# Kernel tuning notes

Measured on AMD Instinct MI355X. Metric: run time of the kernel, lower is better.

## Reference

```python
import jax, jax.numpy as jnp
import numpy as np

B, S, D = 8, 2048, 512  # batch, seq_len, input_dim == qk_dim
K_SIZE = 6


def setup_inputs() -> dict:
    key = jax.random.key(0)
    ks = jax.random.split(key, 8)
    return {
        "evo_local": jax.random.normal(ks[0], (B, S, D), dtype=jnp.float32),
        "Wq": jax.random.normal(ks[1], (D, D), dtype=jnp.float32) * (1.0 / np.sqrt(D)),
        "bq": jax.random.normal(ks[2], (D,), dtype=jnp.float32) * 0.02,
        "dw_w": jax.random.normal(ks[3], (D, 1, K_SIZE), dtype=jnp.float32) * 0.1,  # depthwise conv (O, I/groups=1, K)
        "dw_b": jax.random.normal(ks[4], (D,), dtype=jnp.float32) * 0.02,
        "pw_w": jax.random.normal(ks[5], (D, D), dtype=jnp.float32) * (1.0 / np.sqrt(D)),  # pointwise 1x1 conv as matrix
        "pw_b": jax.random.normal(ks[6], (D,), dtype=jnp.float32) * 0.02,
        "pos": jax.random.normal(ks[7], (1, S, D), dtype=jnp.float32),
    }


def reference(evo_local, Wq, bq, dw_w, dw_b, pw_w, pw_b, pos):
    d = evo_local.shape[-1]
    # Q = Linear(evo_local) + learned positional encoding
    Q = jnp.einsum("bsd,ed->bse", evo_local, Wq) + bq + pos  # [B,S,D]

    # depthwise conv1d, kernel=6, torch padding='same' for even kernel -> pad (2, 3)
    x = jnp.transpose(evo_local, (0, 2, 1))  # [B,D,S]
    kv = jax.lax.conv_general_dilated(
        x, dw_w,
        window_strides=(1,),
        padding=[(2, 3)],
        feature_group_count=d,
        dimension_numbers=("NCH", "OIH", "NCH"),
    ) + dw_b[None, :, None]  # [B,D,S]
    # pointwise 1x1 conv
    kv = jnp.einsum("od,bds->bos", pw_w, kv) + pw_b[None, :, None]  # [B,D,S]
    KV = jnp.transpose(kv, (0, 2, 1))  # [B,S,D]; K and V share this

    scale = 1.0 / jnp.sqrt(jnp.float32(d))
    scores = jnp.einsum("bsd,btd->bst", Q, KV) * scale  # [B,S,S]
    attn = jax.nn.softmax(scores, axis=-1)
    out = jnp.einsum("bst,btd->bsd", attn, KV)
    return out + KV + evo_local
```

## Files before the change

kernel.cpp:

```cpp
#include <hip/hip_runtime.h>


typedef unsigned short ushort_t;
typedef __attribute__((ext_vector_type(8))) short short8;
typedef __attribute__((ext_vector_type(8))) unsigned short u16x8;
typedef __attribute__((ext_vector_type(4))) float f32x4;
typedef float4 f4;

__device__ __forceinline__ float bf2f(ushort_t h) {
    union { unsigned u; float f; } v; v.u = ((unsigned)h) << 16; return v.f;
}
__device__ __forceinline__ ushort_t f2bf(float f) {
    union { float f; unsigned u; } v; v.f = f;
    unsigned r = (v.u + 0x7FFFu + ((v.u >> 16) & 1u)) >> 16;
    return (ushort_t)r;
}

__device__ __forceinline__ void gld_lds16(const void* g, void* l) {
    __builtin_amdgcn_global_load_lds((const __attribute__((address_space(1))) void*)g,
                                     (__attribute__((address_space(3))) void*)l, 16, 0, 0);
}

#define BAR()   asm volatile("s_barrier" ::: "memory")
#define WAITV8  do { asm volatile("s_waitcnt vmcnt(8)" ::: "memory"); __builtin_amdgcn_sched_barrier(0); } while (0)
#define WAITV0  do { asm volatile("s_waitcnt vmcnt(0)" ::: "memory"); __builtin_amdgcn_sched_barrier(0); } while (0)
#define WAITL   do { asm volatile("s_waitcnt lgkmcnt(0)" ::: "memory"); __builtin_amdgcn_sched_barrier(0); } while (0)

template<int EPI>
__global__ __launch_bounds__(512, 2)
void mfma_nt256(const ushort_t* __restrict__ A, long long sA, int ldA,
                const ushort_t* __restrict__ B, long long sB, int ldB,
                int N, int K, float alpha,
                ushort_t* __restrict__ Ch, long long sC,
                float* __restrict__ Cf,
                const ushort_t* __restrict__ addH, const ushort_t* __restrict__ addL,
                const float* __restrict__ addF, long long sAdd)
{
    __shared__ __align__(16) ushort_t lds[65536];

    const int t = threadIdx.x;
    const int w = t >> 6, lane = t & 63;
    const int z = blockIdx.z;
    A += (long long)z * sA;
    B += (long long)z * sB;
    const int m0 = blockIdx.y * 256, n0 = blockIdx.x * 256;
    const int wr = w >> 2, wc = w & 3;
    const int fr = lane & 15, kg = lane >> 4;
    const int nkt = K >> 6;

    const int sRo = lane >> 2;
    const long long sCk = ((lane & 3) ^ ((lane >> 3) & 3)) * 8;
    const int co = (kg ^ ((fr >> 1) & 3)) * 8;

#define STAGE(P, base0, ld, segbase, h, Ts) do {                                         \
    const long long kk_ = (long long)(((Ts) < nkt ? (Ts) : (nkt - 1)) * 64 + (h) * 32) + sCk; \
    const int g0_ = w * 2;                                                               \
    gld_lds16((P) + (long long)((base0) + g0_ * 16 + sRo) * (ld) + kk_,                  \
              &lds[(segbase) + g0_ * 512]);                                              \
    gld_lds16((P) + (long long)((base0) + g0_ * 16 + 16 + sRo) * (ld) + kk_,             \
              &lds[(segbase) + g0_ * 512 + 512]);                                        \
} while (0)

#define AREAD(ksseg) do {                                                                \
    const int ab_ = (ksseg) * 8192 + wr * 4096 + fr * 32 + co;                           \
    _Pragma("unroll") for (int fm_ = 0; fm_ < 8; ++fm_)                                  \
        afr[fm_] = *(const short8*)&lds[ab_ + fm_ * 512];                                \
} while (0)

#define BREAD(ksseg, fnh) do {                                                           \
    const int bb_ = 32768 + (ksseg) * 8192 + wc * 2048 + (fnh) * 1024 + fr * 32 + co;    \
    bfr[0] = *(const short8*)&lds[bb_];                                                  \
    bfr[1] = *(const short8*)&lds[bb_ + 512];                                            \
} while (0)

#define MF2(j0) do {                                                                     \
    __builtin_amdgcn_s_setprio(1);                                                       \
    _Pragma("unroll") for (int fm_ = 0; fm_ < 8; ++fm_) {                                \
        acc[fm_][(j0)]     = __builtin_amdgcn_mfma_f32_16x16x32_bf16(afr[fm_], bfr[0], acc[fm_][(j0)], 0, 0, 0);     \
        acc[fm_][(j0) + 1] = __builtin_amdgcn_mfma_f32_16x16x32_bf16(afr[fm_], bfr[1], acc[fm_][(j0) + 1], 0, 0, 0); \
    }                                                                                    \
    __builtin_amdgcn_s_setprio(0);                                                       \
} while (0)

    const f32x4 zero = {0.f, 0.f, 0.f, 0.f};
    f32x4 acc[8][4];
#pragma unroll
    for (int i = 0; i < 8; ++i)
#pragma unroll
        for (int j = 0; j < 4; ++j) acc[i][j] = zero;

    short8 afr[8], bfr[2];

    STAGE(A, m0, ldA, 0,             0, 0);
    STAGE(B, n0, ldB, 32768,         0, 0);
    STAGE(A, m0, ldA, 8192,          1, 0);
    STAGE(B, n0, ldB, 32768 + 8192,  1, 0);
    STAGE(A, m0, ldA, 16384,         0, 1);
    STAGE(B, n0, ldB, 32768 + 16384, 0, 1);
    WAITV8;
    BAR();

    for (int kt = 0; kt < nkt; ++kt) {
        const int b = kt & 1, nb = b ^ 1;
        AREAD(b * 2); BREAD(b * 2, 0);
        STAGE(A, m0, ldA, (nb * 2 + 1) * 8192, 1, kt + 1);
        BAR(); WAITL;
        MF2(0);
        BAR();
        BREAD(b * 2, 1);
        STAGE(B, n0, ldB, 32768 + (nb * 2 + 1) * 8192, 1, kt + 1);
        BAR(); WAITL;
        MF2(2);
        WAITV8;
        BAR();
        AREAD(b * 2 + 1); BREAD(b * 2 + 1, 0);
        STAGE(A, m0, ldA, (b * 2) * 8192, 0, kt + 2);
        BAR(); WAITL;
        MF2(0);
        BAR();
        BREAD(b * 2 + 1, 1);
        STAGE(B, n0, ldB, 32768 + (b * 2) * 8192, 0, kt + 2);
        BAR(); WAITL;
        MF2(2);
        WAITV8;
        BAR();
    }
    WAITV0;

#pragma unroll
    for (int fm = 0; fm < 8; ++fm)
#pragma unroll
    for (int fn = 0; fn < 4; ++fn)
#pragma unroll
    for (int r = 0; r < 4; ++r) {
        const int m = m0 + wr * 128 + fm * 16 + kg * 4 + r;
        const int n = n0 + wc * 64 + fn * 16 + fr;
        float v = acc[fm][fn][r];
        const long long idx = (long long)m * N + n;
        if (EPI == 2) {
            Ch[(long long)z * sC + idx] = f2bf(v * alpha);
        } else {
            const long long o = (long long)z * sAdd + idx;
            v += bf2f(addH[o]) + bf2f(addL[o]) + addF[o];
            Cf[o] = v;
        }
    }
#undef STAGE
#undef AREAD
#undef BREAD
#undef MF2
}

template<int AF32, int EPI>
__global__ __launch_bounds__(256)
void mfma_nt(const void* __restrict__ Aptr, long long sA, int ldA,
             const ushort_t* __restrict__ Bh, long long sB, int ldB,
             int N, int K, float alpha,
             const float* __restrict__ bias, const float* __restrict__ pos,
             ushort_t* __restrict__ Ch, ushort_t* __restrict__ Cl, ushort_t* __restrict__ CTh,
             long long sC)
{
    __shared__ __align__(16) ushort_t lds[8192];
    ushort_t* lAh = lds;
    ushort_t* lBh = lds + 4096;

    const int t = threadIdx.x;
    const int w = t >> 6, lane = t & 63;
    const int z = blockIdx.z;
    const ushort_t* Ab = (const ushort_t*)Aptr + (long long)z * sA;
    const float*    Af = (const float*)Aptr    + (long long)z * sA;
    Bh += (long long)z * sB;

    const int m0 = blockIdx.y * 128, n0 = blockIdx.x * 128;
    const int wr = w >> 1, wc = w & 1;
    const int fr = lane & 15, kg = lane >> 4;
    const int srow = lane >> 2;
    const int scol = (lane & 3) * 8;

    const f32x4 zero = {0.f, 0.f, 0.f, 0.f};
    f32x4 acc[4][4];
#pragma unroll
    for (int i = 0; i < 4; ++i)
#pragma unroll
        for (int j = 0; j < 4; ++j) acc[i][j] = zero;

    for (int k0 = 0; k0 < K; k0 += 32) {
#pragma unroll
        for (int i = 0; i < 2; ++i) {
            const int g = w * 2 + i;
            const int row = g * 16 + srow;
            if (AF32) {
                const float* p = Af + (long long)(m0 + row) * ldA + k0 + scol;
                f4 v0 = *(const f4*)p;
                f4 v1 = *(const f4*)(p + 4);
                u16x8 o;
                o[0] = f2bf(v0.x); o[1] = f2bf(v0.y); o[2] = f2bf(v0.z); o[3] = f2bf(v0.w);
                o[4] = f2bf(v1.x); o[5] = f2bf(v1.y); o[6] = f2bf(v1.z); o[7] = f2bf(v1.w);
                *(u16x8*)&lAh[g * 512 + srow * 32 + scol] = o;
            } else {
                gld_lds16(Ab + (long long)(m0 + row) * ldA + k0 + scol, &lAh[g * 512]);
            }
            gld_lds16(Bh + (long long)(n0 + row) * ldB + k0 + scol, &lBh[g * 512]);
        }
        __syncthreads();

        short8 aH[4];
#pragma unroll
        for (int fm = 0; fm < 4; ++fm)
            aH[fm] = *(const short8*)&lAh[(wr * 64 + fm * 16 + fr) * 32 + kg * 8];
#pragma unroll
        for (int fn = 0; fn < 4; ++fn) {
            short8 bH = *(const short8*)&lBh[(wc * 64 + fn * 16 + fr) * 32 + kg * 8];
#pragma unroll
            for (int fm = 0; fm < 4; ++fm)
                acc[fm][fn] = __builtin_amdgcn_mfma_f32_16x16x32_bf16(aH[fm], bH, acc[fm][fn], 0, 0, 0);
        }
        __syncthreads();
    }

#pragma unroll
    for (int fm = 0; fm < 4; ++fm)
#pragma unroll
    for (int fn = 0; fn < 4; ++fn)
#pragma unroll
    for (int r = 0; r < 4; ++r) {
        const int m = m0 + wr * 64 + fm * 16 + kg * 4 + r;
        const int n = n0 + wc * 64 + fn * 16 + fr;
        float v = acc[fm][fn][r];
        const long long idx = (long long)m * N + n;
        if (EPI == 0) {
            v += bias[n] + pos[(long long)(m & 2047) * N + n];
            Ch[idx] = f2bf(v);
        } else {
            v += bias[n];
            ushort_t hi = f2bf(v);
            Ch[idx] = hi;
            Cl[idx] = f2bf(v - bf2f(hi));
            CTh[(long long)(m >> 11) * (512LL * 2048) + (long long)n * 2048 + (m & 2047)] = hi;
        }
    }
}

__global__ __launch_bounds__(256)
void cvt2_bf16(const float* __restrict__ a, ushort_t* __restrict__ ao,
               const float* __restrict__ b, ushort_t* __restrict__ bo)
{
    int i = blockIdx.x * 256 + threadIdx.x;
    const float* src = (i < 65536) ? a : b;
    ushort_t* dst = (i < 65536) ? ao : bo;
    int j = i & 65535;
    f4 v = *(const f4*)(src + (long long)j * 4);
    ushort4 o;
    o.x = f2bf(v.x); o.y = f2bf(v.y); o.z = f2bf(v.z); o.w = f2bf(v.w);
    *(ushort4*)&dst[(long long)j * 4] = o;
}

__global__ __launch_bounds__(256)
void dwconv_bf16(const float* __restrict__ x, const float* __restrict__ w,
                 const float* __restrict__ bias, ushort_t* __restrict__ y)
{
    const int tid = blockIdx.x * 256 + threadIdx.x;
    const int d4 = tid & 127;
    const int rest = tid >> 7;
    const int sc = rest & 255;
    const int b = rest >> 8;
    const int s0 = sc * 8;
    const float* xb = x + ((long long)b * 2048) * 512 + d4 * 4;

    f4 win[13];
#pragma unroll
    for (int j = 0; j < 13; ++j) {
        int r = s0 + j - 2;
        int rc = r < 0 ? 0 : (r > 2047 ? 2047 : r);
        f4 v = *(const f4*)(xb + (long long)rc * 512);
        if (r < 0 || r > 2047) { v.x = 0.f; v.y = 0.f; v.z = 0.f; v.w = 0.f; }
        win[j] = v;
    }
    float wk[4][6];
#pragma unroll
    for (int dd = 0; dd < 4; ++dd)
#pragma unroll
        for (int k = 0; k < 6; ++k) wk[dd][k] = w[(d4 * 4 + dd) * 6 + k];
    const f4 bs4 = *(const f4*)(bias + d4 * 4);

    ushort_t* yb = y + ((long long)b * 2048 + s0) * 512 + d4 * 4;
#pragma unroll
    for (int u = 0; u < 8; ++u) {
        float a0 = bs4.x, a1 = bs4.y, a2 = bs4.z, a3 = bs4.w;
#pragma unroll
        for (int k = 0; k < 6; ++k) {
            f4 v = win[u + k];
            a0 = fmaf(v.x, wk[0][k], a0);
            a1 = fmaf(v.y, wk[1][k], a1);
            a2 = fmaf(v.z, wk[2][k], a2);
            a3 = fmaf(v.w, wk[3][k], a3);
        }
        ushort4 o;
        o.x = f2bf(a0); o.y = f2bf(a1); o.z = f2bf(a2); o.w = f2bf(a3);
        *(ushort4*)(yb + (long long)u * 512) = o;
    }
}

__global__ __launch_bounds__(256)
void softmax_bf16(ushort_t* __restrict__ p)
{
    ushort_t* row = p + ((long long)blockIdx.x << 11);
    const int t = threadIdx.x;
    __shared__ float redMax[4];
    __shared__ float redSum[4];

    u16x8 u = *(const u16x8*)(row + t * 8);
    float x[8];
#pragma unroll
    for (int i = 0; i < 8; ++i) x[i] = bf2f(u[i]);

    float m = x[0];
#pragma unroll
    for (int i = 1; i < 8; ++i) m = fmaxf(m, x[i]);
#pragma unroll
    for (int off = 32; off > 0; off >>= 1) m = fmaxf(m, __shfl_xor(m, off));
    if ((t & 63) == 0) redMax[t >> 6] = m;
    __syncthreads();
    m = fmaxf(fmaxf(redMax[0], redMax[1]), fmaxf(redMax[2], redMax[3]));

    float e[8], s = 0.f;
#pragma unroll
    for (int i = 0; i < 8; ++i) { e[i] = __expf(x[i] - m); s += e[i]; }
#pragma unroll
    for (int off = 32; off > 0; off >>= 1) s += __shfl_xor(s, off);
    if ((t & 63) == 0) redSum[t >> 6] = s;
    __syncthreads();
    s = (redSum[0] + redSum[1]) + (redSum[2] + redSum[3]);
    const float inv = 1.0f / s;

#pragma unroll
    for (int i = 0; i < 8; ++i) u[i] = f2bf(e[i] * inv);
    *(u16x8*)(row + t * 8) = u;
}

extern "C" void kernel_launch(void* const* d_in, const int* in_sizes, int n_in,
                              void* d_out, int out_size, void* d_ws, size_t ws_size,
                              hipStream_t stream)
{
    const float* evo  = (const float*)d_in[0];
    const float* Wq   = (const float*)d_in[1];
    const float* bq   = (const float*)d_in[2];
    const float* dw_w = (const float*)d_in[3];
    const float* dw_b = (const float*)d_in[4];
    const float* pw_w = (const float*)d_in[5];
    const float* pw_b = (const float*)d_in[6];
    const float* pos  = (const float*)d_in[7];
    float* out = (float*)d_out;

    const long long BSD = 8LL * 2048 * 512;
    const long long DD  = 512LL * 512;
    const long long SD  = 2048LL * 512;
    const long long SS  = 2048LL * 2048;

    ushort_t* QHi  = (ushort_t*)d_ws;
    ushort_t* KVHi = QHi + BSD;
    ushort_t* KVLo = KVHi + BSD;
    ushort_t* KVT  = KVLo + BSD;
    ushort_t* WqB  = KVT + BSD;
    ushort_t* pwB  = WqB + DD;
    ushort_t* X    = pwB + DD;

    long long Xbytes = (long long)ws_size - 68157440LL;
    long long cRaw = Xbytes / (SS * 2);
    int c;
    if (cRaw >= 8) c = 8; else if (cRaw >= 4) c = 4; else if (cRaw >= 2) c = 2; else c = 1;

    ushort_t* dwout = X;

    cvt2_bf16<<<512, 256, 0, stream>>>(Wq, WqB, pw_w, pwB);
    dwconv_bf16<<<1024, 256, 0, stream>>>(evo, dw_w, dw_b, dwout);

    mfma_nt<1, 0><<<dim3(4, 128, 1), 256, 0, stream>>>(
        evo, 0LL, 512, WqB, 0LL, 512, 512, 512, 1.f,
        bq, pos, QHi, nullptr, nullptr, 0LL);

    mfma_nt<0, 1><<<dim3(4, 128, 1), 256, 0, stream>>>(
        dwout, 0LL, 512, pwB, 0LL, 512, 512, 512, 1.f,
        pw_b, nullptr, KVHi, KVLo, KVT, 0LL);

    const float scale = 0.04419417382415922f;
    for (int b0 = 0; b0 < 8; b0 += c) {
        const int cc = (8 - b0 < c) ? (8 - b0) : c;
        const long long o = (long long)b0 * SD;
        mfma_nt256<2><<<dim3(8, 8, cc), 512, 0, stream>>>(
            QHi + o, SD, 512, KVHi + o, SD, 512, 2048, 512, scale,
            X, SS, nullptr, nullptr, nullptr, nullptr, 0LL);
        softmax_bf16<<<cc * 2048, 256, 0, stream>>>(X);
        mfma_nt256<3><<<dim3(2, 8, cc), 512, 0, stream>>>(
            X, SS, 2048, KVT + o, SD, 2048, 512, 2048, 1.f,
            nullptr, 0LL, out + o, KVHi + o, KVLo + o, evo + o, SD);
    }
}
```

Before: 304.2 us.

## Drop KV low-part residual buffer and remap 256-tile blocks across XCDs

Removes the bf16 low-part (KVLo) of the KV projection, so the pointwise GEMM no longer writes it and the PV epilogue no longer reads it. The residual add now uses only the bf16-rounded KV, which loses some precision. Separately, the big tiled GEMM kernels remap their linear block index so that tiles sharing A/B rows land on the same XCD (QK^T) or run in a different order (PV). The aim is better L2 reuse on the multi-die chip.

```diff
diff --git a/kernel.cpp b/kernel.cpp
--- a/kernel.cpp
+++ b/kernel.cpp
@@ -33,17 +33,33 @@
                 int N, int K, float alpha,
                 ushort_t* __restrict__ Ch, long long sC,
                 float* __restrict__ Cf,
-                const ushort_t* __restrict__ addH, const ushort_t* __restrict__ addL,
+                const ushort_t* __restrict__ addH,
                 const float* __restrict__ addF, long long sAdd)
 {
     __shared__ __align__(16) ushort_t lds[65536];
 
     const int t = threadIdx.x;
     const int w = t >> 6, lane = t & 63;
-    const int z = blockIdx.z;
+
+    int tx, ty, z;
+    if (EPI == 2) {
+        const int lin = blockIdx.x + (blockIdx.y << 3) + (blockIdx.z << 6);
+        const int xcd = lin & 7;
+        const int s   = lin >> 3;
+        z  = s >> 3;
+        const int j = s & 7;
+        ty = 2 * (xcd & 3) + (j >> 2);
+        tx = 4 * (xcd >> 2) + (j & 3);
+    } else {
+        const int lin = blockIdx.x + (blockIdx.y << 1) + (blockIdx.z << 4);
+        ty = lin & 7;
+        tx = (lin >> 3) & 1;
+        z  = lin >> 4;
+    }
     A += (long long)z * sA;
     B += (long long)z * sB;
-    const int m0 = blockIdx.y * 256, n0 = blockIdx.x * 256;
+    const int m0 = ty * 256, n0 = tx * 256;
+
     const int wr = w >> 2, wc = w & 3;
     const int fr = lane & 15, kg = lane >> 4;
     const int nkt = K >> 6;
@@ -141,7 +157,7 @@
             Ch[(long long)z * sC + idx] = f2bf(v * alpha);
         } else {
             const long long o = (long long)z * sAdd + idx;
-            v += bf2f(addH[o]) + bf2f(addL[o]) + addF[o];
+            v += bf2f(addH[o]) + addF[o];
             Cf[o] = v;
         }
     }
@@ -157,7 +173,7 @@
              const ushort_t* __restrict__ Bh, long long sB, int ldB,
              int N, int K, float alpha,
              const float* __restrict__ bias, const float* __restrict__ pos,
-             ushort_t* __restrict__ Ch, ushort_t* __restrict__ Cl, ushort_t* __restrict__ CTh,
+             ushort_t* __restrict__ Ch, ushort_t* __restrict__ CTh,
              long long sC)
 {
     __shared__ __align__(16) ushort_t lds[8192];
@@ -235,7 +251,6 @@
             v += bias[n];
             ushort_t hi = f2bf(v);
             Ch[idx] = hi;
-            Cl[idx] = f2bf(v - bf2f(hi));
             CTh[(long long)(m >> 11) * (512LL * 2048) + (long long)n * 2048 + (m & 2047)] = hi;
         }
     }
@@ -359,13 +374,12 @@
 
     ushort_t* QHi  = (ushort_t*)d_ws;
     ushort_t* KVHi = QHi + BSD;
-    ushort_t* KVLo = KVHi + BSD;
-    ushort_t* KVT  = KVLo + BSD;
+    ushort_t* KVT  = KVHi + BSD;
     ushort_t* WqB  = KVT + BSD;
     ushort_t* pwB  = WqB + DD;
     ushort_t* X    = pwB + DD;
 
-    long long Xbytes = (long long)ws_size - 68157440LL;
+    long long Xbytes = (long long)ws_size - 51380224LL;
     long long cRaw = Xbytes / (SS * 2);
     int c;
     if (cRaw >= 8) c = 8; else if (cRaw >= 4) c = 4; else if (cRaw >= 2) c = 2; else c = 1;
@@ -377,11 +391,11 @@
 
     mfma_nt<1, 0><<<dim3(4, 128, 1), 256, 0, stream>>>(
         evo, 0LL, 512, WqB, 0LL, 512, 512, 512, 1.f,
-        bq, pos, QHi, nullptr, nullptr, 0LL);
+        bq, pos, QHi, nullptr, 0LL);
 
     mfma_nt<0, 1><<<dim3(4, 128, 1), 256, 0, stream>>>(
         dwout, 0LL, 512, pwB, 0LL, 512, 512, 512, 1.f,
-        pw_b, nullptr, KVHi, KVLo, KVT, 0LL);
+        pw_b, nullptr, KVHi, KVT, 0LL);
 
     const float scale = 0.04419417382415922f;
     for (int b0 = 0; b0 < 8; b0 += c) {
@@ -389,10 +403,10 @@
         const long long o = (long long)b0 * SD;
         mfma_nt256<2><<<dim3(8, 8, cc), 512, 0, stream>>>(
             QHi + o, SD, 512, KVHi + o, SD, 512, 2048, 512, scale,
-            X, SS, nullptr, nullptr, nullptr, nullptr, 0LL);
+            X, SS, nullptr, nullptr, nullptr, 0LL);
         softmax_bf16<<<cc * 2048, 256, 0, stream>>>(X);
         mfma_nt256<3><<<dim3(2, 8, cc), 512, 0, stream>>>(
             X, SS, 2048, KVT + o, SD, 2048, 512, 2048, 1.f,
-            nullptr, 0LL, out + o, KVHi + o, KVLo + o, evo + o, SD);
-    }
-}
+            nullptr, 0LL, out + o, KVHi + o, evo + o, SD);
+    }
+}
```

After: 284.7 us. -6.4%, faster.
